# Kernel optimization log

Hardware: AMD Instinct MI355X
Metric: run time of the kernel (lower is better)

Reference implementation:

```python
import jax, jax.numpy as jnp
import numpy as np

N = 50000      # nodes
E = 800000     # edges (avg degree 16)
D = 128        # in_channels
H = 128        # hidden_channels


def sage_conv(x, edge_index, W_l, b_l, W_r):
    """PyG SAGEConv with aggr='mean': lin_l(mean_j x_j) + lin_r(x_i).
    edge_index[0] = source (j), edge_index[1] = destination (i)."""
    src, dst = edge_index[0], edge_index[1]
    n = x.shape[0]
    msg = x[src]                                               # [E, D] gather
    agg = jax.ops.segment_sum(msg, dst, num_segments=n)        # [N, D] scatter-sum
    cnt = jax.ops.segment_sum(jnp.ones((src.shape[0],), x.dtype), dst, num_segments=n)
    agg = agg / jnp.maximum(cnt, 1.0)[:, None]                 # mean (0 for isolated nodes)
    return agg @ W_l.T + b_l + x @ W_r.T


def setup_inputs() -> dict:
    key = jax.random.key(0)
    ks = jax.random.split(key, 9)
    s_in = 1.0 / np.sqrt(D)
    s_h = 1.0 / np.sqrt(H)
    return {
        "x": jax.random.normal(ks[0], (N, D), dtype=jnp.float32),
        "edge_index": jax.random.randint(ks[1], (2, E), 0, N, dtype=jnp.int64),
        "W1l": jax.random.uniform(ks[2], (H, D), jnp.float32, -s_in, s_in),
        "b1l": jnp.zeros((H,), jnp.float32),
        "W1r": jax.random.uniform(ks[3], (H, D), jnp.float32, -s_in, s_in),
        "W2l": jax.random.uniform(ks[4], (H, H), jnp.float32, -s_h, s_h),
        "b2l": jnp.zeros((H,), jnp.float32),
        "W2r": jax.random.uniform(ks[5], (H, H), jnp.float32, -s_h, s_h),
        "W3l": jax.random.uniform(ks[6], (H, H), jnp.float32, -s_h, s_h),
        "b3l": jnp.zeros((H,), jnp.float32),
        "W3r": jax.random.uniform(ks[7], (H, H), jnp.float32, -s_h, s_h),
    }


def reference(x, edge_index, W1l, b1l, W1r, W2l, b2l, W2r, W3l, b3l, W3r):
    x1 = sage_conv(x, edge_index, W1l, b1l, W1r)
    x1 = jax.nn.relu(x1)  # Dropout(0.5) treated as identity (eval mode)
    h_ = sage_conv(x1, edge_index, W2l, b2l, W2r)
    h = sage_conv(x1, edge_index, W3l, b3l, W3r)
    return (h_, h)
```

## Files before the change

### kernel.cpp

```cpp
#include <hip/hip_runtime.h>
#include <stdint.h>
#include <math.h>

typedef __attribute__((ext_vector_type(8))) short short8;
typedef __attribute__((ext_vector_type(4))) float float4v;

__device__ __forceinline__ uint16_t f2bf(float f){
  union { float f; uint32_t i; } c; c.f = f;
  uint32_t r = c.i + 0x7fffu + ((c.i >> 16) & 1u);
  return (uint16_t)(r >> 16);
}
__device__ __forceinline__ uint32_t pack2(float lo, float hi){
  return (uint32_t)f2bf(lo) | ((uint32_t)f2bf(hi) << 16);
}
__device__ __forceinline__ void acc_bf2(uint32_t w, float& x, float& y){
  union { uint32_t i; float f; } a, b;
  a.i = w << 16; b.i = w & 0xffff0000u;
  x += a.f; y += b.f;
}
__device__ __forceinline__ void accum8(uint4 v, float* a){
  acc_bf2(v.x, a[0], a[1]); acc_bf2(v.y, a[2], a[3]);
  acc_bf2(v.z, a[4], a[5]); acc_bf2(v.w, a[6], a[7]);
}


#define P1_EPT 8

__global__ __launch_bounds__(512) void prep_kernel(
    const int* __restrict__ ei, int E, int NB, int CAP,
    int* __restrict__ fill, uint32_t* __restrict__ bins, int p1blk,
    const float* __restrict__ x,
    const float* __restrict__ w0, const float* __restrict__ w1,
    const float* __restrict__ w2, const float* __restrict__ w3,
    const float* __restrict__ w4, const float* __restrict__ w5,
    uint16_t* __restrict__ xb, uint16_t* __restrict__ wb, int nx){
  if ((int)blockIdx.x < p1blk){
    __shared__ int hist[256], base[256], cur[256];
    int tid = threadIdx.x;
    if (tid < 256){ hist[tid] = 0; cur[tid] = 0; }
    __syncthreads();
    int src[P1_EPT], dst[P1_EPT];
    int e0 = blockIdx.x * (512 * P1_EPT);
    #pragma unroll
    for (int k = 0; k < P1_EPT; ++k){
      int e = e0 + k * 512 + tid;
      bool ok = e < E;
      src[k] = ok ? ei[e] : 0;
      dst[k] = ok ? ei[E + e] : -1;
      if (ok) atomicAdd(&hist[dst[k] >> 8], 1);
    }
    __syncthreads();
    if (tid < NB && hist[tid] > 0) base[tid] = atomicAdd(&fill[tid], hist[tid]);
    __syncthreads();
    #pragma unroll
    for (int k = 0; k < P1_EPT; ++k){
      if (dst[k] >= 0){
        int b = dst[k] >> 8;
        int loc = base[b] + atomicAdd(&cur[b], 1);
        if (loc < CAP)
          __builtin_nontemporal_store(
              (uint32_t)src[k] | ((uint32_t)(dst[k] & 255) << 16),
              bins + (size_t)b * CAP + loc);
      }
    }
  } else {
    int i = (blockIdx.x - p1blk) * 512 + threadIdx.x;
    int stride = (gridDim.x - p1blk) * 512;
    for (int j = i; j < (nx >> 2); j += stride){
      float4 v = ((const float4*)x)[j];
      uint2 o;
      o.x = pack2(v.x, v.y); o.y = pack2(v.z, v.w);
      ((uint2*)xb)[j] = o;
    }
    const int WSZ = 128 * 128;
    for (int j = i; j < 6 * WSZ; j += stride){
      int t = j >> 14, o = j & (WSZ - 1);
      const float* w = t == 0 ? w0 : t == 1 ? w1 : t == 2 ? w2 : t == 3 ? w3 : t == 4 ? w4 : w5;
      wb[j] = f2bf(w[o]);
    }
  }
}


__global__ __launch_bounds__(512) void build_kernel(const uint32_t* __restrict__ bins,
                                                    const int* __restrict__ fill,
                                                    int CAP, int n,
                                                    int2* __restrict__ rowptr2,
                                                    uint16_t* __restrict__ esrc){
  __shared__ int h[256], s[256], cursor[256];
  int b = blockIdx.x, tid = threadIdx.x;
  int cnt = fill[b]; if (cnt > CAP) cnt = CAP;
  int gbase = b * CAP;
  if (tid < 256) h[tid] = 0;
  __syncthreads();
  for (int i = tid; i < cnt; i += 512){
    uint32_t v = __builtin_nontemporal_load(bins + (size_t)gbase + i);
    atomicAdd(&h[(v >> 16) & 255], 1);
  }
  __syncthreads();
  if (tid < 256) s[tid] = h[tid];
  __syncthreads();
  #pragma unroll
  for (int off = 1; off < 256; off <<= 1){
    int v = 0;
    if (tid < 256 && tid >= off) v = s[tid - off];
    __syncthreads();
    if (tid < 256) s[tid] += v;
    __syncthreads();
  }
  if (tid < 256){
    int node = (b << 8) + tid;
    int excl = s[tid] - h[tid];
    if (node < n) rowptr2[node] = make_int2(gbase + excl, gbase + s[tid]);
    cursor[tid] = gbase + excl;
  }
  __syncthreads();
  for (int i = tid; i < cnt; i += 512){
    uint32_t v = __builtin_nontemporal_load(bins + (size_t)gbase + i);
    int p = atomicAdd(&cursor[(v >> 16) & 255], 1);
    esrc[p] = (uint16_t)(v & 0xffffu);
  }
}


__global__ __launch_bounds__(256) void agg_kernel(const uint16_t* __restrict__ xin,
                                                  const int2* __restrict__ rowptr2,
                                                  const uint16_t* __restrict__ esrc,
                                                  uint16_t* __restrict__ aggw, int n){
  int node = blockIdx.x * 4 + (threadIdx.x >> 6);
  if (node >= n) return;
  int lane = threadIdx.x & 63;
  int sub = lane >> 4, fq = lane & 15;
  const uint4* xv = (const uint4*)xin;
  int2 be = rowptr2[node];
  int beg = be.x, end = be.y;
  float inv = 1.f / fmaxf((float)(end - beg), 1.f);
  float a[8] = {0.f,0.f,0.f,0.f,0.f,0.f,0.f,0.f};
  int e = beg + sub;
  for (; e + 12 < end; e += 16){
    int s0 = esrc[e], s1 = esrc[e + 4], s2 = esrc[e + 8], s3 = esrc[e + 12];
    uint4 v0 = xv[(size_t)s0 * 16 + fq];
    uint4 v1 = xv[(size_t)s1 * 16 + fq];
    uint4 v2 = xv[(size_t)s2 * 16 + fq];
    uint4 v3 = xv[(size_t)s3 * 16 + fq];
    accum8(v0, a); accum8(v1, a); accum8(v2, a); accum8(v3, a);
  }
  for (; e < end; e += 4){
    uint4 v = xv[(size_t)esrc[e] * 16 + fq];
    accum8(v, a);
  }
  #pragma unroll
  for (int i = 0; i < 8; ++i){
    a[i] += __shfl_xor(a[i], 16);
    a[i] += __shfl_xor(a[i], 32);
    a[i] *= inv;
  }
  if (sub == 0){
    uint4 o;
    o.x = pack2(a[0], a[1]); o.y = pack2(a[2], a[3]);
    o.z = pack2(a[4], a[5]); o.w = pack2(a[6], a[7]);
    ((uint4*)aggw)[(size_t)node * 16 + fq] = o;
  }
}


#define WT_STRIDE 136

__device__ __forceinline__ void stage_weights(const uint16_t* __restrict__ Wl,
                                              const uint16_t* __restrict__ Wr,
                                              int ch, uint16_t* lds_l,
                                              uint16_t* lds_r, int tid){
  const uint4* srcL = (const uint4*)(Wl + (size_t)(ch * 64) * 128);
  const uint4* srcR = (const uint4*)(Wr + (size_t)(ch * 64) * 128);
  #pragma unroll
  for (int i = 0; i < 4; ++i){
    int j = tid + i * 256;
    int row = j >> 4, c8 = j & 15;
    uint4 vl = srcL[j], vr = srcR[j];
    *(uint4*)(lds_l + row * WT_STRIDE + c8 * 8) = vl;
    *(uint4*)(lds_r + row * WT_STRIDE + c8 * 8) = vr;
  }
}

__global__ __launch_bounds__(256) void gemm1_kernel(
    const uint16_t* __restrict__ Aagg, const uint16_t* __restrict__ Ax,
    const uint16_t* __restrict__ Wl, const uint16_t* __restrict__ Wr,
    const float* __restrict__ bias, uint16_t* __restrict__ x1b, int n){
  __shared__ uint16_t lds_l[64 * WT_STRIDE], lds_r[64 * WT_STRIDE];
  int tid = threadIdx.x, lane = tid & 63, wid = tid >> 6;
  int m = lane & 15, quad = lane >> 4;
  int r0 = blockIdx.x * 64 + wid * 16;
  int arow = r0 + m; if (arow > n - 1) arow = n - 1;

  short8 a0f[4], a1f[4];
  #pragma unroll
  for (int ks = 0; ks < 4; ++ks){
    a0f[ks] = *(const short8*)(Aagg + (size_t)arow * 128 + ks * 32 + quad * 8);
    a1f[ks] = *(const short8*)(Ax   + (size_t)arow * 128 + ks * 32 + quad * 8);
  }

  for (int ch = 0; ch < 2; ++ch){
    if (ch) __syncthreads();
    stage_weights(Wl, Wr, ch, lds_l, lds_r, tid);
    __syncthreads();
    float4v acc[4];
    #pragma unroll
    for (int ct = 0; ct < 4; ++ct) acc[ct] = (float4v){0.f, 0.f, 0.f, 0.f};
    #pragma unroll
    for (int ks = 0; ks < 4; ++ks){
      #pragma unroll
      for (int ct = 0; ct < 4; ++ct){
        short8 b0 = *(const short8*)(lds_l + (ct * 16 + m) * WT_STRIDE + ks * 32 + quad * 8);
        acc[ct] = __builtin_amdgcn_mfma_f32_16x16x32_bf16(a0f[ks], b0, acc[ct], 0, 0, 0);
        short8 b1 = *(const short8*)(lds_r + (ct * 16 + m) * WT_STRIDE + ks * 32 + quad * 8);
        acc[ct] = __builtin_amdgcn_mfma_f32_16x16x32_bf16(a1f[ks], b1, acc[ct], 0, 0, 0);
      }
    }
    #pragma unroll
    for (int ct = 0; ct < 4; ++ct){
      int col = ch * 64 + ct * 16 + m;
      float bv = bias[col];
      #pragma unroll
      for (int i = 0; i < 4; ++i){
        int grow = r0 + quad * 4 + i;
        if (grow < n)
          x1b[(size_t)grow * 128 + col] = f2bf(fmaxf(acc[ct][i] + bv, 0.f));
      }
    }
  }
}

__global__ __launch_bounds__(256) void gemm23_kernel(
    const uint16_t* __restrict__ Aagg, const uint16_t* __restrict__ Ax,
    const uint16_t* __restrict__ W2l, const uint16_t* __restrict__ W2r,
    const float* __restrict__ b2,
    const uint16_t* __restrict__ W3l, const uint16_t* __restrict__ W3r,
    const float* __restrict__ b3,
    float* __restrict__ out, size_t half, int n){
  __shared__ uint16_t lds_l[64 * WT_STRIDE], lds_r[64 * WT_STRIDE];
  int tid = threadIdx.x, lane = tid & 63, wid = tid >> 6;
  int m = lane & 15, quad = lane >> 4;
  int r0 = blockIdx.x * 64 + wid * 16;
  int arow = r0 + m; if (arow > n - 1) arow = n - 1;

  short8 a0f[4], a1f[4];
  #pragma unroll
  for (int ks = 0; ks < 4; ++ks){
    a0f[ks] = *(const short8*)(Aagg + (size_t)arow * 128 + ks * 32 + quad * 8);
    a1f[ks] = *(const short8*)(Ax   + (size_t)arow * 128 + ks * 32 + quad * 8);
  }

  for (int idx = 0; idx < 4; ++idx){
    int pass = idx >> 1, ch = idx & 1;
    if (idx) __syncthreads();
    stage_weights(pass ? W3l : W2l, pass ? W3r : W2r, ch, lds_l, lds_r, tid);
    __syncthreads();
    float4v acc[4];
    #pragma unroll
    for (int ct = 0; ct < 4; ++ct) acc[ct] = (float4v){0.f, 0.f, 0.f, 0.f};
    #pragma unroll
    for (int ks = 0; ks < 4; ++ks){
      #pragma unroll
      for (int ct = 0; ct < 4; ++ct){
        short8 b0 = *(const short8*)(lds_l + (ct * 16 + m) * WT_STRIDE + ks * 32 + quad * 8);
        acc[ct] = __builtin_amdgcn_mfma_f32_16x16x32_bf16(a0f[ks], b0, acc[ct], 0, 0, 0);
        short8 b1 = *(const short8*)(lds_r + (ct * 16 + m) * WT_STRIDE + ks * 32 + quad * 8);
        acc[ct] = __builtin_amdgcn_mfma_f32_16x16x32_bf16(a1f[ks], b1, acc[ct], 0, 0, 0);
      }
    }
    const float* bb = pass ? b3 : b2;
    float* op = out + (pass ? half : 0);
    #pragma unroll
    for (int ct = 0; ct < 4; ++ct){
      int col = ch * 64 + ct * 16 + m;
      float bv = bb[col];
      #pragma unroll
      for (int i = 0; i < 4; ++i){
        int grow = r0 + quad * 4 + i;
        if (grow < n) op[(size_t)grow * 128 + col] = acc[ct][i] + bv;
      }
    }
  }
}


extern "C" void kernel_launch(void* const* d_in, const int* in_sizes, int n_in,
                              void* d_out, int out_size, void* d_ws, size_t ws_size,
                              hipStream_t stream) {
  const float* x   = (const float*)d_in[0];
  const int*   ei  = (const int*)d_in[1];
  const float* W1l = (const float*)d_in[2];
  const float* b1l = (const float*)d_in[3];
  const float* W1r = (const float*)d_in[4];
  const float* W2l = (const float*)d_in[5];
  const float* b2l = (const float*)d_in[6];
  const float* W2r = (const float*)d_in[7];
  const float* W3l = (const float*)d_in[8];
  const float* b3l = (const float*)d_in[9];
  const float* W3r = (const float*)d_in[10];
  float* out = (float*)d_out;

  const int n = in_sizes[0] / 128;
  const int E = in_sizes[1] / 2;
  const size_t half = (size_t)n * 128;
  const int WSZ = 128 * 128;

  const int NB = (n + 255) >> 8;
  int mean = (E + NB - 1) / NB;
  int CAP = mean + 8 * (int)sqrt((double)mean) + 64;
  CAP = (CAP + 63) & ~63;

  size_t off = 0;
  auto carve = [&](size_t bytes) -> void* {
    void* p = (char*)d_ws + off;
    off += (bytes + 255) & ~(size_t)255;
    return p;
  };
  int2*     rowptr2 = (int2*)carve((size_t)n * 8);
  int*      fill    = (int*)carve((size_t)NB * 4);
  uint16_t* esrc    = (uint16_t*)carve((size_t)NB * CAP * 2);
  uint16_t* xb      = (uint16_t*)carve(half * 2);
  uint16_t* wb      = (uint16_t*)carve((size_t)6 * WSZ * 2);
  uint16_t* x1b     = (uint16_t*)carve(half * 2);
  uint16_t* agg     = (uint16_t*)carve(half * 2);
  uint32_t* bins    = (uint32_t*)carve((size_t)NB * CAP * 4);
  (void)ws_size;

  hipMemsetAsync(fill, 0, (size_t)NB * 4, stream);

  int p1blk = (E + 512 * P1_EPT - 1) / (512 * P1_EPT);
  int cblk  = 256;
  prep_kernel<<<p1blk + cblk, 512, 0, stream>>>(ei, E, NB, CAP, fill, bins, p1blk,
                                                x, W1l, W1r, W2l, W2r, W3l, W3r,
                                                xb, wb, (int)half);
  build_kernel<<<NB, 512, 0, stream>>>(bins, fill, CAP, n, rowptr2, esrc);

  int ablk = (n + 3) / 4;
  int gblk = (n + 63) / 64;
  const uint16_t *Wb1l = wb, *Wb1r = wb + WSZ, *Wb2l = wb + 2 * WSZ,
                 *Wb2r = wb + 3 * WSZ, *Wb3l = wb + 4 * WSZ, *Wb3r = wb + 5 * WSZ;

  agg_kernel<<<ablk, 256, 0, stream>>>(xb, rowptr2, esrc, agg, n);
  gemm1_kernel<<<gblk, 256, 0, stream>>>(agg, xb, Wb1l, Wb1r, b1l, x1b, n);

  agg_kernel<<<ablk, 256, 0, stream>>>(x1b, rowptr2, esrc, agg, n);
  gemm23_kernel<<<gblk, 256, 0, stream>>>(agg, x1b, Wb2l, Wb2r, b2l,
                                          Wb3l, Wb3r, b3l, out, half, n);
}
```

Measured before the change: 229.2 us.

## Replace bucketed binning CSR build with degree count, scan, atomic scatter

Builds the destination-sorted CSR with three steps: a global atomic degree histogram, a single-block prefix scan over a padded 65536-node degree array, and a per-edge atomic scatter of 32-bit source indices. This drops the two-pass shared-memory bucketing and the per-bucket capacity over-allocation. In exchange it uses global atomics on hot counters, a serial single-block scan, and twice the edge index width in the aggregation reads. It also hardcodes a node limit of 65536.

```diff
diff --git a/kernel.cpp b/kernel.cpp
--- a/kernel.cpp
+++ b/kernel.cpp
@@ -24,48 +24,22 @@
 }
 
 
-#define P1_EPT 8
-
-__global__ __launch_bounds__(512) void prep_kernel(
-    const int* __restrict__ ei, int E, int NB, int CAP,
-    int* __restrict__ fill, uint32_t* __restrict__ bins, int p1blk,
+__global__ __launch_bounds__(256) void prep_kernel(
+    const int* __restrict__ ei, int E, int cntblk,
+    int* __restrict__ deg,
     const float* __restrict__ x,
     const float* __restrict__ w0, const float* __restrict__ w1,
     const float* __restrict__ w2, const float* __restrict__ w3,
     const float* __restrict__ w4, const float* __restrict__ w5,
     uint16_t* __restrict__ xb, uint16_t* __restrict__ wb, int nx){
-  if ((int)blockIdx.x < p1blk){
-    __shared__ int hist[256], base[256], cur[256];
-    int tid = threadIdx.x;
-    if (tid < 256){ hist[tid] = 0; cur[tid] = 0; }
-    __syncthreads();
-    int src[P1_EPT], dst[P1_EPT];
-    int e0 = blockIdx.x * (512 * P1_EPT);
-    #pragma unroll
-    for (int k = 0; k < P1_EPT; ++k){
-      int e = e0 + k * 512 + tid;
-      bool ok = e < E;
-      src[k] = ok ? ei[e] : 0;
-      dst[k] = ok ? ei[E + e] : -1;
-      if (ok) atomicAdd(&hist[dst[k] >> 8], 1);
-    }
-    __syncthreads();
-    if (tid < NB && hist[tid] > 0) base[tid] = atomicAdd(&fill[tid], hist[tid]);
-    __syncthreads();
-    #pragma unroll
-    for (int k = 0; k < P1_EPT; ++k){
-      if (dst[k] >= 0){
-        int b = dst[k] >> 8;
-        int loc = base[b] + atomicAdd(&cur[b], 1);
-        if (loc < CAP)
-          __builtin_nontemporal_store(
-              (uint32_t)src[k] | ((uint32_t)(dst[k] & 255) << 16),
-              bins + (size_t)b * CAP + loc);
-      }
-    }
+  if ((int)blockIdx.x < cntblk){
+    int i = blockIdx.x * 256 + threadIdx.x;
+    int stride = cntblk * 256;
+    for (int e = i; e < E; e += stride)
+      atomicAdd(&deg[ei[E + e]], 1);
   } else {
-    int i = (blockIdx.x - p1blk) * 512 + threadIdx.x;
-    int stride = (gridDim.x - p1blk) * 512;
+    int i = (blockIdx.x - cntblk) * 256 + threadIdx.x;
+    int stride = (gridDim.x - cntblk) * 256;
     for (int j = i; j < (nx >> 2); j += stride){
       float4 v = ((const float4*)x)[j];
       uint2 o;
@@ -82,58 +56,66 @@
 }
 
 
-__global__ __launch_bounds__(512) void build_kernel(const uint32_t* __restrict__ bins,
-                                                    const int* __restrict__ fill,
-                                                    int CAP, int n,
-                                                    int2* __restrict__ rowptr2,
-                                                    uint16_t* __restrict__ esrc){
-  __shared__ int h[256], s[256], cursor[256];
-  int b = blockIdx.x, tid = threadIdx.x;
-  int cnt = fill[b]; if (cnt > CAP) cnt = CAP;
-  int gbase = b * CAP;
-  if (tid < 256) h[tid] = 0;
+__global__ __launch_bounds__(1024) void scan_kernel(const int* __restrict__ deg,
+                                                    int n,
+                                                    int* __restrict__ rowptr,
+                                                    int* __restrict__ cursor){
+  __shared__ int part[1024];
+  int tid = threadIdx.x;
+  int4 v[16];
+  #pragma unroll
+  for (int k = 0; k < 16; ++k) v[k] = ((const int4*)deg)[tid * 16 + k];
+  int s = 0;
+  #pragma unroll
+  for (int k = 0; k < 16; ++k) s += v[k].x + v[k].y + v[k].z + v[k].w;
+  part[tid] = s;
   __syncthreads();
-  for (int i = tid; i < cnt; i += 512){
-    uint32_t v = __builtin_nontemporal_load(bins + (size_t)gbase + i);
-    atomicAdd(&h[(v >> 16) & 255], 1);
-  }
-  __syncthreads();
-  if (tid < 256) s[tid] = h[tid];
-  __syncthreads();
-  #pragma unroll
-  for (int off = 1; off < 256; off <<= 1){
-    int v = 0;
-    if (tid < 256 && tid >= off) v = s[tid - off];
+  for (int off = 1; off < 1024; off <<= 1){
+    int t = (tid >= off) ? part[tid - off] : 0;
     __syncthreads();
-    if (tid < 256) s[tid] += v;
+    part[tid] += t;
     __syncthreads();
   }
-  if (tid < 256){
-    int node = (b << 8) + tid;
-    int excl = s[tid] - h[tid];
-    if (node < n) rowptr2[node] = make_int2(gbase + excl, gbase + s[tid]);
-    cursor[tid] = gbase + excl;
-  }
-  __syncthreads();
-  for (int i = tid; i < cnt; i += 512){
-    uint32_t v = __builtin_nontemporal_load(bins + (size_t)gbase + i);
-    int p = atomicAdd(&cursor[(v >> 16) & 255], 1);
-    esrc[p] = (uint16_t)(v & 0xffffu);
+  int run = part[tid] - s;
+  int base = tid * 64;
+  #pragma unroll
+  for (int k = 0; k < 16; ++k){
+    int d[4] = { v[k].x, v[k].y, v[k].z, v[k].w };
+    #pragma unroll
+    for (int q = 0; q < 4; ++q){
+      int i = base + k * 4 + q;
+      if (i < n){ rowptr[i] = run; cursor[i] = run; }
+      run += d[q];
+    }
+  }
+  if (tid == 1023) rowptr[n] = part[1023];
+}
+
+
+__global__ __launch_bounds__(256) void scatter_kernel(const int* __restrict__ ei,
+                                                      int E,
+                                                      int* __restrict__ cursor,
+                                                      uint32_t* __restrict__ esrc){
+  int i = blockIdx.x * 256 + threadIdx.x;
+  int stride = gridDim.x * 256;
+  for (int e = i; e < E; e += stride){
+    int s = ei[e], d = ei[E + e];
+    int p = atomicAdd(&cursor[d], 1);
+    esrc[p] = (uint32_t)s;
   }
 }
 
 
 __global__ __launch_bounds__(256) void agg_kernel(const uint16_t* __restrict__ xin,
-                                                  const int2* __restrict__ rowptr2,
-                                                  const uint16_t* __restrict__ esrc,
+                                                  const int* __restrict__ rowptr,
+                                                  const uint32_t* __restrict__ esrc,
                                                   uint16_t* __restrict__ aggw, int n){
   int node = blockIdx.x * 4 + (threadIdx.x >> 6);
   if (node >= n) return;
   int lane = threadIdx.x & 63;
   int sub = lane >> 4, fq = lane & 15;
   const uint4* xv = (const uint4*)xin;
-  int2 be = rowptr2[node];
-  int beg = be.x, end = be.y;
+  int beg = rowptr[node], end = rowptr[node + 1];
   float inv = 1.f / fmaxf((float)(end - beg), 1.f);
   float a[8] = {0.f,0.f,0.f,0.f,0.f,0.f,0.f,0.f};
   int e = beg + sub;
@@ -304,11 +286,7 @@
   const int E = in_sizes[1] / 2;
   const size_t half = (size_t)n * 128;
   const int WSZ = 128 * 128;
-
-  const int NB = (n + 255) >> 8;
-  int mean = (E + NB - 1) / NB;
-  int CAP = mean + 8 * (int)sqrt((double)mean) + 64;
-  CAP = (CAP + 63) & ~63;
+  const int NPAD = 65536;
 
   size_t off = 0;
   auto carve = [&](size_t bytes) -> void* {
@@ -316,34 +294,34 @@
     off += (bytes + 255) & ~(size_t)255;
     return p;
   };
-  int2*     rowptr2 = (int2*)carve((size_t)n * 8);
-  int*      fill    = (int*)carve((size_t)NB * 4);
-  uint16_t* esrc    = (uint16_t*)carve((size_t)NB * CAP * 2);
-  uint16_t* xb      = (uint16_t*)carve(half * 2);
-  uint16_t* wb      = (uint16_t*)carve((size_t)6 * WSZ * 2);
-  uint16_t* x1b     = (uint16_t*)carve(half * 2);
-  uint16_t* agg     = (uint16_t*)carve(half * 2);
-  uint32_t* bins    = (uint32_t*)carve((size_t)NB * CAP * 4);
+  int*      rowptr = (int*)carve((size_t)(n + 1) * 4);
+  int*      deg    = (int*)carve((size_t)NPAD * 4);
+  int*      cursor = (int*)carve((size_t)NPAD * 4);
+  uint32_t* esrc   = (uint32_t*)carve((size_t)E * 4);
+  uint16_t* xb     = (uint16_t*)carve(half * 2);
+  uint16_t* wb     = (uint16_t*)carve((size_t)6 * WSZ * 2);
+  uint16_t* x1b    = (uint16_t*)carve(half * 2);
+  uint16_t* agg    = (uint16_t*)carve(half * 2);
   (void)ws_size;
 
-  hipMemsetAsync(fill, 0, (size_t)NB * 4, stream);
-
-  int p1blk = (E + 512 * P1_EPT - 1) / (512 * P1_EPT);
-  int cblk  = 256;
-  prep_kernel<<<p1blk + cblk, 512, 0, stream>>>(ei, E, NB, CAP, fill, bins, p1blk,
-                                                x, W1l, W1r, W2l, W2r, W3l, W3r,
-                                                xb, wb, (int)half);
-  build_kernel<<<NB, 512, 0, stream>>>(bins, fill, CAP, n, rowptr2, esrc);
+  hipMemsetAsync(deg, 0, (size_t)NPAD * 4, stream);
+
+  const int cntblk = 256, convblk = 768;
+  prep_kernel<<<cntblk + convblk, 256, 0, stream>>>(ei, E, cntblk, deg,
+                                                    x, W1l, W1r, W2l, W2r, W3l, W3r,
+                                                    xb, wb, (int)half);
+  scan_kernel<<<1, 1024, 0, stream>>>(deg, n, rowptr, cursor);
+  scatter_kernel<<<1024, 256, 0, stream>>>(ei, E, cursor, esrc);
 
   int ablk = (n + 3) / 4;
   int gblk = (n + 63) / 64;
   const uint16_t *Wb1l = wb, *Wb1r = wb + WSZ, *Wb2l = wb + 2 * WSZ,
                  *Wb2r = wb + 3 * WSZ, *Wb3l = wb + 4 * WSZ, *Wb3r = wb + 5 * WSZ;
 
-  agg_kernel<<<ablk, 256, 0, stream>>>(xb, rowptr2, esrc, agg, n);
+  agg_kernel<<<ablk, 256, 0, stream>>>(xb, rowptr, esrc, agg, n);
   gemm1_kernel<<<gblk, 256, 0, stream>>>(agg, xb, Wb1l, Wb1r, b1l, x1b, n);
 
-  agg_kernel<<<ablk, 256, 0, stream>>>(x1b, rowptr2, esrc, agg, n);
+  agg_kernel<<<ablk, 256, 0, stream>>>(x1b, rowptr, esrc, agg, n);
   gemm23_kernel<<<gblk, 256, 0, stream>>>(agg, x1b, Wb2l, Wb2r, b2l,
                                           Wb3l, Wb3r, b3l, out, half, n);
 }
```

Result: slower. 344.4 us (+50.2%).

## Stage edge binning and CSR build in LDS for coalesced stores

Applied to the files above, without the earlier changes.

The edge-binning pass now sorts each block's 4096 edges by bucket in shared memory with a local prefix scan, then writes them out contiguously per bucket. Before, each edge was scattered straight to global memory. The CSR build likewise sorts source indices in LDS and streams them out with coalesced nontemporal stores, and esrc widens from uint16 to uint32. Final output writes become nontemporal and the conversion grid doubles. This adds LDS use, limiting occupancy, and caps CAP and per-bucket counts at 5120. The wider esrc doubles its memory footprint and read traffic in the aggregation kernel.

```diff
diff --git a/kernel.cpp b/kernel.cpp
--- a/kernel.cpp
+++ b/kernel.cpp
@@ -24,44 +24,65 @@
 }
 
 
-#define P1_EPT 8
-
 __global__ __launch_bounds__(512) void prep_kernel(
-    const int* __restrict__ ei, int E, int NB, int CAP,
-    int* __restrict__ fill, uint32_t* __restrict__ bins, int p1blk,
+    const int* __restrict__ ei, int E, int NB, int CAP, int p1blk,
+    int* __restrict__ fill, uint32_t* __restrict__ bins,
     const float* __restrict__ x,
     const float* __restrict__ w0, const float* __restrict__ w1,
     const float* __restrict__ w2, const float* __restrict__ w3,
     const float* __restrict__ w4, const float* __restrict__ w5,
     uint16_t* __restrict__ xb, uint16_t* __restrict__ wb, int nx){
   if ((int)blockIdx.x < p1blk){
-    __shared__ int hist[256], base[256], cur[256];
+    __shared__ int hist[256], scn[256], cursor[256], gbase[256], excl[256];
+    __shared__ uint32_t stage[4096];
     int tid = threadIdx.x;
-    if (tid < 256){ hist[tid] = 0; cur[tid] = 0; }
-    __syncthreads();
-    int src[P1_EPT], dst[P1_EPT];
-    int e0 = blockIdx.x * (512 * P1_EPT);
-    #pragma unroll
-    for (int k = 0; k < P1_EPT; ++k){
+    if (tid < 256) hist[tid] = 0;
+    __syncthreads();
+    int e0 = blockIdx.x * 4096;
+    int nval = E - e0; if (nval > 4096) nval = 4096;
+    uint32_t w[8]; int bk[8];
+    #pragma unroll
+    for (int k = 0; k < 8; ++k){
       int e = e0 + k * 512 + tid;
       bool ok = e < E;
-      src[k] = ok ? ei[e] : 0;
-      dst[k] = ok ? ei[E + e] : -1;
-      if (ok) atomicAdd(&hist[dst[k] >> 8], 1);
-    }
-    __syncthreads();
-    if (tid < NB && hist[tid] > 0) base[tid] = atomicAdd(&fill[tid], hist[tid]);
-    __syncthreads();
-    #pragma unroll
-    for (int k = 0; k < P1_EPT; ++k){
-      if (dst[k] >= 0){
-        int b = dst[k] >> 8;
-        int loc = base[b] + atomicAdd(&cur[b], 1);
-        if (loc < CAP)
-          __builtin_nontemporal_store(
-              (uint32_t)src[k] | ((uint32_t)(dst[k] & 255) << 16),
-              bins + (size_t)b * CAP + loc);
-      }
+      int s = ok ? ei[e] : 0;
+      int d = ok ? ei[E + e] : 0;
+      w[k] = (uint32_t)s | ((uint32_t)d << 16);
+      bk[k] = ok ? (d >> 8) : -1;
+      if (ok) atomicAdd(&hist[bk[k]], 1);
+    }
+    __syncthreads();
+    if (tid < 256) scn[tid] = hist[tid];
+    __syncthreads();
+    #pragma unroll
+    for (int off = 1; off < 256; off <<= 1){
+      int v = 0;
+      if (tid < 256 && tid >= off) v = scn[tid - off];
+      __syncthreads();
+      if (tid < 256) scn[tid] += v;
+      __syncthreads();
+    }
+    if (tid < 256){
+      int ex = scn[tid] - hist[tid];
+      excl[tid] = ex; cursor[tid] = ex;
+      gbase[tid] = (tid < NB && hist[tid] > 0)
+                   ? atomicAdd(&fill[tid], hist[tid]) : 0;
+    }
+    __syncthreads();
+    #pragma unroll
+    for (int k = 0; k < 8; ++k){
+      if (bk[k] >= 0){
+        int p = atomicAdd(&cursor[bk[k]], 1);
+        stage[p] = w[k];
+      }
+    }
+    __syncthreads();
+    for (int i = tid; i < nval; i += 512){
+      uint32_t v = stage[i];
+      int b = v >> 24;
+      int loc = gbase[b] + (i - excl[b]);
+      if (loc < CAP)
+        __builtin_nontemporal_store(v, bins + (size_t)b * CAP + loc);
     }
   } else {
     int i = (blockIdx.x - p1blk) * 512 + threadIdx.x;
@@ -86,46 +107,48 @@
                                                     const int* __restrict__ fill,
                                                     int CAP, int n,
                                                     int2* __restrict__ rowptr2,
-                                                    uint16_t* __restrict__ esrc){
-  __shared__ int h[256], s[256], cursor[256];
+                                                    uint32_t* __restrict__ esrc){
+  __shared__ int hist[256], scn[256], cursor[256], excl[256];
+  __shared__ uint32_t stage[5120];
   int b = blockIdx.x, tid = threadIdx.x;
-  int cnt = fill[b]; if (cnt > CAP) cnt = CAP;
-  int gbase = b * CAP;
-  if (tid < 256) h[tid] = 0;
-  __syncthreads();
-  for (int i = tid; i < cnt; i += 512){
-    uint32_t v = __builtin_nontemporal_load(bins + (size_t)gbase + i);
-    atomicAdd(&h[(v >> 16) & 255], 1);
-  }
-  __syncthreads();
-  if (tid < 256) s[tid] = h[tid];
+  int cnt = fill[b]; if (cnt > CAP) cnt = CAP; if (cnt > 5120) cnt = 5120;
+  size_t gb = (size_t)b * CAP;
+  if (tid < 256) hist[tid] = 0;
+  __syncthreads();
+  for (int i = tid; i < cnt; i += 512)
+    atomicAdd(&hist[(bins[gb + i] >> 16) & 255], 1);
+  __syncthreads();
+  if (tid < 256) scn[tid] = hist[tid];
   __syncthreads();
   #pragma unroll
   for (int off = 1; off < 256; off <<= 1){
     int v = 0;
-    if (tid < 256 && tid >= off) v = s[tid - off];
-    __syncthreads();
-    if (tid < 256) s[tid] += v;
+    if (tid < 256 && tid >= off) v = scn[tid - off];
+    __syncthreads();
+    if (tid < 256) scn[tid] += v;
     __syncthreads();
   }
   if (tid < 256){
+    int ex = scn[tid] - hist[tid];
+    excl[tid] = ex; cursor[tid] = ex;
     int node = (b << 8) + tid;
-    int excl = s[tid] - h[tid];
-    if (node < n) rowptr2[node] = make_int2(gbase + excl, gbase + s[tid]);
-    cursor[tid] = gbase + excl;
+    if (node < n) rowptr2[node] = make_int2((int)gb + ex, (int)gb + scn[tid]);
   }
   __syncthreads();
   for (int i = tid; i < cnt; i += 512){
-    uint32_t v = __builtin_nontemporal_load(bins + (size_t)gbase + i);
+    uint32_t v = bins[gb + i];
     int p = atomicAdd(&cursor[(v >> 16) & 255], 1);
-    esrc[p] = (uint16_t)(v & 0xffffu);
-  }
+    stage[p] = v & 0xffffu;
+  }
+  __syncthreads();
+  for (int i = tid; i < cnt; i += 512)
+    __builtin_nontemporal_store(stage[i], esrc + gb + i);
 }
 
 
 __global__ __launch_bounds__(256) void agg_kernel(const uint16_t* __restrict__ xin,
                                                   const int2* __restrict__ rowptr2,
-                                                  const uint16_t* __restrict__ esrc,
+                                                  const uint32_t* __restrict__ esrc,
                                                   uint16_t* __restrict__ aggw, int n){
   int node = blockIdx.x * 4 + (threadIdx.x >> 6);
   if (node >= n) return;
@@ -277,7 +300,9 @@
       #pragma unroll
       for (int i = 0; i < 4; ++i){
         int grow = r0 + quad * 4 + i;
-        if (grow < n) op[(size_t)grow * 128 + col] = acc[ct][i] + bv;
+        if (grow < n)
+          __builtin_nontemporal_store(acc[ct][i] + bv,
+                                      op + (size_t)grow * 128 + col);
       }
     }
   }
@@ -309,6 +334,7 @@
   int mean = (E + NB - 1) / NB;
   int CAP = mean + 8 * (int)sqrt((double)mean) + 64;
   CAP = (CAP + 63) & ~63;
+  if (CAP > 5120) CAP = 5120;
 
   size_t off = 0;
   auto carve = [&](size_t bytes) -> void* {
@@ -318,7 +344,7 @@
   };
   int2*     rowptr2 = (int2*)carve((size_t)n * 8);
   int*      fill    = (int*)carve((size_t)NB * 4);
-  uint16_t* esrc    = (uint16_t*)carve((size_t)NB * CAP * 2);
+  uint32_t* esrc    = (uint32_t*)carve((size_t)NB * CAP * 4);
   uint16_t* xb      = (uint16_t*)carve(half * 2);
   uint16_t* wb      = (uint16_t*)carve((size_t)6 * WSZ * 2);
   uint16_t* x1b     = (uint16_t*)carve(half * 2);
@@ -328,9 +354,9 @@
 
   hipMemsetAsync(fill, 0, (size_t)NB * 4, stream);
 
-  int p1blk = (E + 512 * P1_EPT - 1) / (512 * P1_EPT);
-  int cblk  = 256;
-  prep_kernel<<<p1blk + cblk, 512, 0, stream>>>(ei, E, NB, CAP, fill, bins, p1blk,
+  int p1blk = (E + 4095) / 4096;
+  int cblk  = 512;
+  prep_kernel<<<p1blk + cblk, 512, 0, stream>>>(ei, E, NB, CAP, p1blk, fill, bins,
                                                 x, W1l, W1r, W2l, W2r, W3l, W3r,
                                                 xb, wb, (int)half);
   build_kernel<<<NB, 512, 0, stream>>>(bins, fill, CAP, n, rowptr2, esrc);
```

Result: faster. 215.6 us (-6.0%).
